# Kernel optimization log

Hardware: AMD Instinct MI355X
Metric: run time of the kernel (lower is better)

## Reference

```python
import jax, jax.numpy as jnp
import numpy as np

N_HEAD = 16
N_EMBD = 1024
HEAD_DIM = N_EMBD // N_HEAD
ROPE_BASE = 10000.0


def _rms_norm(x):
    # F.rms_norm with eps=None uses dtype eps
    eps = jnp.finfo(x.dtype).eps
    ms = jnp.mean(jnp.square(x), axis=-1, keepdims=True)
    return x * jax.lax.rsqrt(ms + eps)


def _rope_tables(T, dtype):
    inv_freq = 1.0 / (ROPE_BASE ** (jnp.arange(0, HEAD_DIM, 2, dtype=jnp.float32) / HEAD_DIM))
    t = jnp.arange(T, dtype=jnp.float32)
    freqs = jnp.outer(t, inv_freq)  # [T, D/2]
    cos = jnp.cos(freqs).astype(dtype)[None, :, None, :]  # [1,T,1,D/2]
    sin = jnp.sin(freqs).astype(dtype)[None, :, None, :]
    return cos, sin


def _apply_rotary(x, cos, sin):
    d = x.shape[-1] // 2
    x1, x2 = x[..., :d], x[..., d:]
    y1 = x1 * cos + x2 * sin
    y2 = -x1 * sin + x2 * cos
    return jnp.concatenate([y1, y2], axis=-1).astype(x.dtype)


def setup_inputs() -> dict:
    key = jax.random.key(0)
    ks = jax.random.split(key, 7)
    B, T, C = 4, 2048, N_EMBD
    s = 0.02
    return {
        "x": jax.random.normal(ks[0], (B, T, C), dtype=jnp.float32),
        "v1": jax.random.normal(ks[1], (B, T, C), dtype=jnp.float32),
        "Wq": jax.random.normal(ks[2], (C, C), dtype=jnp.float32) * s,
        "Wk": jax.random.normal(ks[3], (C, C), dtype=jnp.float32) * s,
        "Wv": jax.random.normal(ks[4], (C, C), dtype=jnp.float32) * s,
        "Wproj": jax.random.normal(ks[5], (C, C), dtype=jnp.float32) * s,
        "lamb": jnp.float32(0.5),
    }


def reference(x, v1, Wq, Wk, Wv, Wproj, lamb):
    B, T, C = x.shape
    H, D = N_HEAD, HEAD_DIM
    q = (x @ Wq.T).reshape(B, T, H, D)
    k = (x @ Wk.T).reshape(B, T, H, D)
    v = (x @ Wv.T).reshape(B, T, H, D)
    # value-lambda residual mix
    v = (1.0 - lamb) * v + lamb * v1.reshape(B, T, H, D)
    # RMSNorm then RoPE on q, k
    cos, sin = _rope_tables(T, x.dtype)
    q = _apply_rotary(_rms_norm(q), cos, sin)
    k = _apply_rotary(_rms_norm(k), cos, sin)
    # causal SDPA
    scale = 1.0 / jnp.sqrt(jnp.float32(D)).astype(x.dtype)
    scores = jnp.einsum("bthd,bshd->bhts", q, k) * scale  # [B,H,T,T]
    causal = jnp.tril(jnp.ones((T, T), dtype=bool))
    scores = jnp.where(causal[None, None], scores, jnp.finfo(scores.dtype).min)
    attn = jax.nn.softmax(scores, axis=-1)
    y = jnp.einsum("bhts,bshd->bthd", attn, v).reshape(B, T, C)
    y = y @ Wproj.T
    return (y, v1)
```

## Files before the change

kernel.cpp:

```cpp
#include <hip/hip_runtime.h>
#include <hip/hip_bf16.h>

typedef __bf16 bf16x8 __attribute__((ext_vector_type(8)));
typedef __bf16 bf16x4 __attribute__((ext_vector_type(4)));
typedef float  f32x4  __attribute__((ext_vector_type(4)));
typedef unsigned u32x4 __attribute__((ext_vector_type(4)));

#define B_ 4
#define T_ 2048
#define H_ 16
#define D_ 64
#define C_ 1024
#define M_ 8192
#define NE_ ((size_t)M_ * C_)

__global__ void probe_dtype(const unsigned short* __restrict__ x,
                            int* __restrict__ flag)
{
  __shared__ float red[256];
  float m = 0.0f;
  for (int i = threadIdx.x; i < 4096; i += 256) {
    unsigned int u = ((unsigned int)x[i]) << 16;
    float v = fabsf(__uint_as_float(u));
    if (!(v <= 1e30f)) v = 1e31f;
    m = fmaxf(m, v);
  }
  red[threadIdx.x] = m;
  __syncthreads();
  for (int s = 128; s > 0; s >>= 1) {
    if (threadIdx.x < s) red[threadIdx.x] = fmaxf(red[threadIdx.x], red[threadIdx.x + s]);
    __syncthreads();
  }
  if (threadIdx.x == 0) *flag = (red[0] > 100.0f) ? 1 : 0;
}

__device__ __forceinline__ float load1_adapt(const void* p, size_t idx, int f)
{
  if (f) return ((const float*)p)[idx];
  return __bfloat162float(((const __hip_bfloat16*)p)[idx]);
}

__global__ __launch_bounds__(256) void cvt_bf16(
    const int* __restrict__ flagp, const void* __restrict__ src,
    __bf16* __restrict__ dst, int n)
{
  const int f = *flagp;
  for (size_t i = ((size_t)blockIdx.x * 256 + threadIdx.x) * 8; i < (size_t)n;
       i += (size_t)gridDim.x * 2048) {
    bf16x8 r;
    if (f) {
      const float* pf = (const float*)src + i;
      float4 a = *(const float4*)pf;
      float4 b = *(const float4*)(pf + 4);
      r[0] = (__bf16)a.x; r[1] = (__bf16)a.y; r[2] = (__bf16)a.z; r[3] = (__bf16)a.w;
      r[4] = (__bf16)b.x; r[5] = (__bf16)b.y; r[6] = (__bf16)b.z; r[7] = (__bf16)b.w;
    } else {
      r = *(const bf16x8*)((const __bf16*)src + i);
    }
    *(bf16x8*)(dst + i) = r;
  }
}

__device__ __forceinline__ void g2lds16(const __bf16* g, __bf16* l)
{
  __builtin_amdgcn_global_load_lds(
      (const __attribute__((address_space(1))) void*)g,
      (__attribute__((address_space(3))) void*)l, 16, 0, 0);
}

__device__ __forceinline__ unsigned cvtpk_bf16(float lo, float hi)
{
  unsigned r;
  asm("v_cvt_pk_bf16_f32 %0, %1, %2" : "=v"(r) : "v"(lo), "v"(hi));
  return r;
}

__global__ __launch_bounds__(256) void gemm128(
    const __bf16* __restrict__ A, const __bf16* __restrict__ Bm,
    void* __restrict__ C, int M, int N, int K,
    const int* __restrict__ flagp, int adaptive)
{
  __shared__ __bf16 As[128][64];
  __shared__ __bf16 Bs[128][64];

  const int tid  = threadIdx.x;
  const int wv   = tid >> 6;
  const int lane = tid & 63;
  const int n16  = lane & 15;
  const int quad = lane >> 4;
  const int wm = (wv & 1) * 64, wn = (wv >> 1) * 64;

  const int nwgx = gridDim.x;
  const int id   = blockIdx.y * nwgx + blockIdx.x;
  const int cpx  = (nwgx * gridDim.y) >> 3;
  const int swz  = (id & 7) * cpx + (id >> 3);
  const int m0 = (swz % nwgx) * 128, n0 = (swz / nwgx) * 128;

  f32x4 acc[4][4];
#pragma unroll
  for (int i = 0; i < 4; i++)
#pragma unroll
    for (int j = 0; j < 4; j++) acc[i][j] = (f32x4){0.f, 0.f, 0.f, 0.f};

  const int trow = tid >> 3;
  const int tcol = (tid & 7) * 8;

  for (int k0 = 0; k0 < K; k0 += 64) {
#pragma unroll
    for (int p = 0; p < 4; p++) {
      g2lds16(A  + (size_t)(m0 + trow + p * 32) * K + k0 + tcol,
              &As[trow + p * 32][tcol]);
      g2lds16(Bm + (size_t)(n0 + trow + p * 32) * K + k0 + tcol,
              &Bs[trow + p * 32][tcol]);
    }
    __syncthreads();

#pragma unroll
    for (int kk = 0; kk < 2; kk++) {
      bf16x8 af[4], bf[4];
#pragma unroll
      for (int i = 0; i < 4; i++) {
        af[i] = *(const bf16x8*)&As[wm + i * 16 + n16][kk * 32 + quad * 8];
        bf[i] = *(const bf16x8*)&Bs[wn + i * 16 + n16][kk * 32 + quad * 8];
      }
#pragma unroll
      for (int i = 0; i < 4; i++)
#pragma unroll
        for (int j = 0; j < 4; j++)
          acc[i][j] = __builtin_amdgcn_mfma_f32_16x16x32_bf16(af[i], bf[j],
                                                              acc[i][j], 0, 0, 0);
    }
    __syncthreads();
  }

  const int f = adaptive ? *flagp : 0;
  const int rb = quad * 4;
#pragma unroll
  for (int i = 0; i < 4; i++)
#pragma unroll
    for (int j = 0; j < 4; j++)
#pragma unroll
      for (int r = 0; r < 4; r++) {
        const size_t idx = (size_t)(m0 + wm + i * 16 + rb + r) * N
                           + n0 + wn + j * 16 + n16;
        if (f) ((float*)C)[idx] = acc[i][j][r];
        else   ((__bf16*)C)[idx] = (__bf16)acc[i][j][r];
      }
}

__global__ __launch_bounds__(256) void fuse_rope_vmix(
    const int* __restrict__ flagp,
    __hip_bfloat16* __restrict__ q,
    __hip_bfloat16* __restrict__ k,
    __hip_bfloat16* __restrict__ v,
    const void* __restrict__ v1,
    const void* __restrict__ lambp)
{
  const int f    = *flagp;
  const int task = blockIdx.x * 4 + (threadIdx.x >> 6);
  const int lane = threadIdx.x & 63;
  const int h  = task & 15;
  const int bt = task >> 4;
  const int t  = bt & (T_ - 1);
  const size_t base = (size_t)bt * C_ + h * D_ + lane;

  const int j = lane & 31;
  const float inv = expf(-(float)j * (9.2103403719761836f / 32.0f));
  const float ang = (float)t * inv;
  const float cs = cosf(ang), sn = sinf(ang);
  const float EPS = 0.0078125f;

  {
    float xv = __bfloat162float(q[base]);
    float ss = xv * xv;
#pragma unroll
    for (int off = 32; off >= 1; off >>= 1) ss += __shfl_xor(ss, off);
    float r  = rsqrtf(ss * (1.0f / 64.0f) + EPS);
    float xn = xv * r;
    float pr = __shfl_xor(xn, 32);
    float yv = (lane < 32) ? (xn * cs + pr * sn) : (pr * -sn + xn * cs);
    q[base] = __float2bfloat16(yv);
  }
  {
    float xv = __bfloat162float(k[base]);
    float ss = xv * xv;
#pragma unroll
    for (int off = 32; off >= 1; off >>= 1) ss += __shfl_xor(ss, off);
    float r  = rsqrtf(ss * (1.0f / 64.0f) + EPS);
    float xn = xv * r;
    float pr = __shfl_xor(xn, 32);
    float yv = (lane < 32) ? (xn * cs + pr * sn) : (pr * -sn + xn * cs);
    k[base] = __float2bfloat16(yv);
  }
  {
    float lam = load1_adapt(lambp, 0, f);
    float vv  = __bfloat162float(v[base]);
    float v1v = load1_adapt(v1, base, f);
    v[base] = __float2bfloat16((1.0f - lam) * vv + lam * v1v);
  }
}

__global__ __launch_bounds__(256) void transp_v(
    const __bf16* __restrict__ v, __bf16* __restrict__ vt)
{
  __shared__ __bf16 Ts[64][72];
  const int bh = blockIdx.y;
  const int t0 = blockIdx.x * 64;
  const int b = bh >> 4, h = bh & 15;

  const int r = threadIdx.x >> 2;
  const int c = (threadIdx.x & 3) * 16;
  const __bf16* src = v + (size_t)(b * T_ + t0 + r) * C_ + h * D_ + c;
  *(bf16x8*)&Ts[r][c]     = *(const bf16x8*)src;
  *(bf16x8*)&Ts[r][c + 8] = *(const bf16x8*)(src + 8);
  __syncthreads();

  const int d  = threadIdx.x >> 2;
  const int tc = (threadIdx.x & 3) * 16;
  bf16x8 o0, o1;
#pragma unroll
  for (int jj = 0; jj < 8; jj++) { o0[jj] = Ts[tc + jj][d]; o1[jj] = Ts[tc + 8 + jj][d]; }
  __bf16* dst = vt + (size_t)(bh * D_ + d) * T_ + t0 + tc;
  *(bf16x8*)dst       = o0;
  *(bf16x8*)(dst + 8) = o1;
}

__global__ __launch_bounds__(256, 3) void attn_mfma(
    const __bf16* q,
    const __bf16* __restrict__ k,
    const __bf16* __restrict__ vt,
    __bf16* y)
{
  const int tid  = threadIdx.x;
  const int wv   = tid >> 6;
  const int lane = tid & 63;
  const int n16  = lane & 15;
  const int quad = lane >> 4;

  const int id = blockIdx.y * gridDim.x + blockIdx.x;
  const int bh = (id & 7) + 8 * ((id >> 3) & 7);
  const int bx = id >> 6;
  const int b = bh >> 4, h = bh & 15;
  const int q0 = (gridDim.x - 1 - bx) * 128;
  const size_t hb  = (size_t)b * T_ * C_ + h * D_;
  const size_t vhb = (size_t)bh * D_ * T_;

  bf16x8 aq[2][2];
#pragma unroll
  for (int rt = 0; rt < 2; rt++) {
    const size_t qoff = hb + (size_t)(q0 + wv * 32 + rt * 16 + n16) * C_;
    aq[rt][0] = *(const bf16x8*)(q + qoff + quad * 8);
    aq[rt][1] = *(const bf16x8*)(q + qoff + 32 + quad * 8);
#pragma unroll
    for (int jj = 0; jj < 8; jj++) {
      aq[rt][0][jj] = (__bf16)((float)aq[rt][0][jj] * 0.125f);
      aq[rt][1][jj] = (__bf16)((float)aq[rt][1][jj] * 0.125f);
    }
  }

  f32x4 Ot[2][4];
  float l_lane[2];
#pragma unroll
  for (int rt = 0; rt < 2; rt++) {
    l_lane[rt] = 0.0f;
#pragma unroll
    for (int t = 0; t < 4; t++) Ot[rt][t] = (f32x4){0.f, 0.f, 0.f, 0.f};
  }

  const int srcA = n16 + 32 * (quad & 1);
  const int srcB = srcA + 16;
  const bool lowq = quad < 2;

  const int rbase0 = q0 + wv * 32;
  const int niter  = (rbase0 + 31) / 64 + 1;

  for (int it = 0; it < niter; it++) {
    const int s0 = it * 64;

    bf16x8 kf[4][2], vf[4][2];
#pragma unroll
    for (int t = 0; t < 4; t++) {
      const __bf16* kp = k + hb + (size_t)(s0 + t * 16 + n16) * C_;
      kf[t][0] = *(const bf16x8*)(kp + quad * 8);
      kf[t][1] = *(const bf16x8*)(kp + 32 + quad * 8);
      const __bf16* vp = vt + vhb + (size_t)(t * 16 + n16) * T_ + s0;
      vf[t][0] = *(const bf16x8*)(vp + quad * 8);
      vf[t][1] = *(const bf16x8*)(vp + 32 + quad * 8);
    }

#pragma unroll
    for (int rt = 0; rt < 2; rt++) {
      const int rbase = rbase0 + rt * 16;
      if (s0 <= rbase + 15) {
        f32x4 S[4];
        __builtin_amdgcn_s_setprio(1);
#pragma unroll
        for (int t = 0; t < 4; t++) {
          S[t] = (f32x4){0.f, 0.f, 0.f, 0.f};
          S[t] = __builtin_amdgcn_mfma_f32_16x16x32_bf16(kf[t][0], aq[rt][0], S[t], 0, 0, 0);
          S[t] = __builtin_amdgcn_mfma_f32_16x16x32_bf16(kf[t][1], aq[rt][1], S[t], 0, 0, 0);
        }
        __builtin_amdgcn_s_setprio(0);

        if (s0 + 63 > rbase) {
          const int tg = rbase + n16;
#pragma unroll
          for (int t = 0; t < 4; t++) {
#pragma unroll
            for (int r = 0; r < 4; r++) {
              const int sg = s0 + t * 16 + quad * 4 + r;
              if (sg > tg) S[t][r] = -1e30f;
            }
          }
        }

        float p[4][4];
#pragma unroll
        for (int t = 0; t < 4; t++)
#pragma unroll
          for (int r = 0; r < 4; r++)
            p[t][r] = __expf(S[t][r] - 8.0f);
        l_lane[rt] += ((p[0][0] + p[0][1]) + (p[0][2] + p[0][3]))
                    + ((p[1][0] + p[1][1]) + (p[1][2] + p[1][3]))
                    + ((p[2][0] + p[2][1]) + (p[2][2] + p[2][3]))
                    + ((p[3][0] + p[3][1]) + (p[3][2] + p[3][3]));

        unsigned pk0[4], pk1[4];
#pragma unroll
        for (int t = 0; t < 4; t++) {
          pk0[t] = cvtpk_bf16(p[t][0], p[t][1]);
          pk1[t] = cvtpk_bf16(p[t][2], p[t][3]);
        }

        bf16x8 pf[2];
#pragma unroll
        for (int c = 0; c < 2; c++) {
          const int tE = 2 * c, tO = 2 * c + 1;
          unsigned a0 = (unsigned)__shfl((int)pk0[tE], srcA);
          unsigned a1 = (unsigned)__shfl((int)pk0[tO], srcA);
          unsigned b0 = (unsigned)__shfl((int)pk1[tE], srcA);
          unsigned b1 = (unsigned)__shfl((int)pk1[tO], srcA);
          unsigned c0 = (unsigned)__shfl((int)pk0[tE], srcB);
          unsigned c1 = (unsigned)__shfl((int)pk0[tO], srcB);
          unsigned d0 = (unsigned)__shfl((int)pk1[tE], srcB);
          unsigned d1 = (unsigned)__shfl((int)pk1[tO], srcB);
          union { u32x4 u; bf16x8 bv; } uw;
          uw.u[0] = lowq ? a0 : a1;
          uw.u[1] = lowq ? b0 : b1;
          uw.u[2] = lowq ? c0 : c1;
          uw.u[3] = lowq ? d0 : d1;
          pf[c] = uw.bv;
        }

        __builtin_amdgcn_s_setprio(1);
#pragma unroll
        for (int t = 0; t < 4; t++) {
          Ot[rt][t] = __builtin_amdgcn_mfma_f32_16x16x32_bf16(vf[t][0], pf[0], Ot[rt][t], 0, 0, 0);
          Ot[rt][t] = __builtin_amdgcn_mfma_f32_16x16x32_bf16(vf[t][1], pf[1], Ot[rt][t], 0, 0, 0);
        }
        __builtin_amdgcn_s_setprio(0);
      }
    }
  }

#pragma unroll
  for (int rt = 0; rt < 2; rt++) {
    float lt = l_lane[rt];
    lt += __shfl_xor(lt, 16);
    lt += __shfl_xor(lt, 32);
    const float linv = 1.0f / lt;
    const int qrow = q0 + wv * 32 + rt * 16 + n16;
#pragma unroll
    for (int t = 0; t < 4; t++) {
      bf16x4 o;
#pragma unroll
      for (int r = 0; r < 4; r++) o[r] = (__bf16)(Ot[rt][t][r] * linv);
      *(bf16x4*)(y + hb + (size_t)qrow * C_ + t * 16 + quad * 4) = o;
    }
  }
}

__global__ __launch_bounds__(256) void copy_v1(
    const int* __restrict__ flagp, const void* __restrict__ v1, void* __restrict__ out)
{
  const int f = *flagp;
  const size_t nbytes = NE_ * (f ? 4u : 2u);
  const uint4* s = (const uint4*)v1;
  uint4* d = (uint4*)((char*)out + nbytes);
  const size_t n16 = nbytes / 16;
  for (size_t i = (size_t)blockIdx.x * 256 + threadIdx.x; i < n16;
       i += (size_t)gridDim.x * 256)
    d[i] = s[i];
}

extern "C" void kernel_launch(void* const* d_in, const int* in_sizes, int n_in,
                              void* d_out, int out_size, void* d_ws, size_t ws_size,
                              hipStream_t stream)
{
  const void* x    = d_in[0];
  const void* v1   = d_in[1];
  const void* Wq   = d_in[2];
  const void* Wk   = d_in[3];
  const void* Wv   = d_in[4];
  const void* Wp   = d_in[5];
  const void* lamb = d_in[6];

  __bf16* xb  = (__bf16*)d_ws;
  __bf16* qw  = xb + NE_;
  __bf16* wqb = qw + NE_;
  __bf16* wkb = wqb + (size_t)C_ * C_;
  __bf16* wvb = wkb + (size_t)C_ * C_;
  __bf16* wpb = wvb + (size_t)C_ * C_;
  int* flagp  = (int*)(wpb + (size_t)C_ * C_);
  __bf16* vtb = xb;
  __bf16* kw = (__bf16*)d_out;
  __bf16* vw = (__bf16*)((char*)d_out + NE_ * 2);

  probe_dtype<<<1, 256, 0, stream>>>((const unsigned short*)x, flagp);

  cvt_bf16<<<4096, 256, 0, stream>>>(flagp, x,  xb,  (int)NE_);
  cvt_bf16<<<512,  256, 0, stream>>>(flagp, Wq, wqb, C_ * C_);
  cvt_bf16<<<512,  256, 0, stream>>>(flagp, Wk, wkb, C_ * C_);
  cvt_bf16<<<512,  256, 0, stream>>>(flagp, Wv, wvb, C_ * C_);
  cvt_bf16<<<512,  256, 0, stream>>>(flagp, Wp, wpb, C_ * C_);

  dim3 gg(M_ / 128, C_ / 128);
  gemm128<<<gg, 256, 0, stream>>>(xb, wqb, qw, M_, C_, C_, flagp, 0);
  gemm128<<<gg, 256, 0, stream>>>(xb, wkb, kw, M_, C_, C_, flagp, 0);
  gemm128<<<gg, 256, 0, stream>>>(xb, wvb, vw, M_, C_, C_, flagp, 0);

  fuse_rope_vmix<<<(M_ * H_) / 4, 256, 0, stream>>>(
      flagp, (__hip_bfloat16*)qw, (__hip_bfloat16*)kw, (__hip_bfloat16*)vw,
      v1, lamb);

  transp_v<<<dim3(T_ / 64, B_ * H_), 256, 0, stream>>>(vw, vtb);

  attn_mfma<<<dim3(T_ / 128, B_ * H_), 256, 0, stream>>>(qw, kw, vtb, qw);

  gemm128<<<gg, 256, 0, stream>>>(qw, wpb, d_out, M_, C_, C_, flagp, 1);
  copy_v1<<<8192, 256, 0, stream>>>(flagp, v1, d_out);
}
```

Baseline: 448.7 us.

## Fuse K/V projections into one GEMM and double-buffer attention K/V loads

Wk and Wv are assumed to sit next to each other in the workspace, so one GEMM with N=2048 produces an interleaved KV buffer with row stride 2048. The rope, transpose and attention kernels now index K and V with that stride. The attention loop is rewritten to prefetch the next 64-key K/V tile into a second register set while the current tile is computed, and launch bounds drop from 3 to 2 waves per SIMD to make room for the extra registers. This trades occupancy for load/compute overlap and saves one GEMM launch. It depends on wkb and wvb being contiguous, which holds for the existing workspace layout.

Result: no change. 452.3 us (+0.8%).

```diff
diff --git a/kernel.cpp b/kernel.cpp
--- a/kernel.cpp
+++ b/kernel.cpp
@@ -13,6 +13,7 @@
 #define C_ 1024
 #define M_ 8192
 #define NE_ ((size_t)M_ * C_)
+#define KVSTR_ 2048
 
 __global__ void probe_dtype(const unsigned short* __restrict__ x,
                             int* __restrict__ flag)
@@ -151,8 +152,7 @@
 __global__ __launch_bounds__(256) void fuse_rope_vmix(
     const int* __restrict__ flagp,
     __hip_bfloat16* __restrict__ q,
-    __hip_bfloat16* __restrict__ k,
-    __hip_bfloat16* __restrict__ v,
+    __hip_bfloat16* __restrict__ kv,
     const void* __restrict__ v1,
     const void* __restrict__ lambp)
 {
@@ -162,7 +162,8 @@
   const int h  = task & 15;
   const int bt = task >> 4;
   const int t  = bt & (T_ - 1);
-  const size_t base = (size_t)bt * C_ + h * D_ + lane;
+  const size_t baseq = (size_t)bt * C_ + h * D_ + lane;
+  const size_t basek = (size_t)bt * KVSTR_ + h * D_ + lane;
 
   const int j = lane & 31;
   const float inv = expf(-(float)j * (9.2103403719761836f / 32.0f));
@@ -171,7 +172,7 @@
   const float EPS = 0.0078125f;
 
   {
-    float xv = __bfloat162float(q[base]);
+    float xv = __bfloat162float(q[baseq]);
     float ss = xv * xv;
 #pragma unroll
     for (int off = 32; off >= 1; off >>= 1) ss += __shfl_xor(ss, off);
@@ -179,10 +180,10 @@
     float xn = xv * r;
     float pr = __shfl_xor(xn, 32);
     float yv = (lane < 32) ? (xn * cs + pr * sn) : (pr * -sn + xn * cs);
-    q[base] = __float2bfloat16(yv);
+    q[baseq] = __float2bfloat16(yv);
   }
   {
-    float xv = __bfloat162float(k[base]);
+    float xv = __bfloat162float(kv[basek]);
     float ss = xv * xv;
 #pragma unroll
     for (int off = 32; off >= 1; off >>= 1) ss += __shfl_xor(ss, off);
@@ -190,18 +191,18 @@
     float xn = xv * r;
     float pr = __shfl_xor(xn, 32);
     float yv = (lane < 32) ? (xn * cs + pr * sn) : (pr * -sn + xn * cs);
-    k[base] = __float2bfloat16(yv);
+    kv[basek] = __float2bfloat16(yv);
   }
   {
     float lam = load1_adapt(lambp, 0, f);
-    float vv  = __bfloat162float(v[base]);
-    float v1v = load1_adapt(v1, base, f);
-    v[base] = __float2bfloat16((1.0f - lam) * vv + lam * v1v);
+    float vv  = __bfloat162float(kv[basek + 1024]);
+    float v1v = load1_adapt(v1, baseq, f);
+    kv[basek + 1024] = __float2bfloat16((1.0f - lam) * vv + lam * v1v);
   }
 }
 
 __global__ __launch_bounds__(256) void transp_v(
-    const __bf16* __restrict__ v, __bf16* __restrict__ vt)
+    const __bf16* __restrict__ kv, __bf16* __restrict__ vt)
 {
   __shared__ __bf16 Ts[64][72];
   const int bh = blockIdx.y;
@@ -210,7 +211,7 @@
 
   const int r = threadIdx.x >> 2;
   const int c = (threadIdx.x & 3) * 16;
-  const __bf16* src = v + (size_t)(b * T_ + t0 + r) * C_ + h * D_ + c;
+  const __bf16* src = kv + (size_t)(b * T_ + t0 + r) * KVSTR_ + 1024 + h * D_ + c;
   *(bf16x8*)&Ts[r][c]     = *(const bf16x8*)src;
   *(bf16x8*)&Ts[r][c + 8] = *(const bf16x8*)(src + 8);
   __syncthreads();
@@ -225,9 +226,89 @@
   *(bf16x8*)(dst + 8) = o1;
 }
 
-__global__ __launch_bounds__(256, 3) void attn_mfma(
+__device__ __forceinline__ void attn_tile(
+    const bf16x8 (&KF)[4][2], const bf16x8 (&VF)[4][2],
+    const bf16x8 (&aq)[2][2], f32x4 (&Ot)[2][4], float (&l_lane)[2],
+    int s0, int rbase0, int n16, int quad, int srcA, int srcB, bool lowq)
+{
+#pragma unroll
+  for (int rt = 0; rt < 2; rt++) {
+    const int rbase = rbase0 + rt * 16;
+    if (s0 <= rbase + 15) {
+      f32x4 S[4];
+      __builtin_amdgcn_s_setprio(1);
+#pragma unroll
+      for (int t = 0; t < 4; t++) {
+        S[t] = (f32x4){0.f, 0.f, 0.f, 0.f};
+        S[t] = __builtin_amdgcn_mfma_f32_16x16x32_bf16(KF[t][0], aq[rt][0], S[t], 0, 0, 0);
+        S[t] = __builtin_amdgcn_mfma_f32_16x16x32_bf16(KF[t][1], aq[rt][1], S[t], 0, 0, 0);
+      }
+      __builtin_amdgcn_s_setprio(0);
+
+      if (s0 + 63 > rbase) {
+        const int tg = rbase + n16;
+#pragma unroll
+        for (int t = 0; t < 4; t++) {
+#pragma unroll
+          for (int r = 0; r < 4; r++) {
+            const int sg = s0 + t * 16 + quad * 4 + r;
+            if (sg > tg) S[t][r] = -1e30f;
+          }
+        }
+      }
+
+      float p[4][4];
+#pragma unroll
+      for (int t = 0; t < 4; t++)
+#pragma unroll
+        for (int r = 0; r < 4; r++)
+          p[t][r] = __expf(S[t][r] - 8.0f);
+      l_lane[rt] += ((p[0][0] + p[0][1]) + (p[0][2] + p[0][3]))
+                  + ((p[1][0] + p[1][1]) + (p[1][2] + p[1][3]))
+                  + ((p[2][0] + p[2][1]) + (p[2][2] + p[2][3]))
+                  + ((p[3][0] + p[3][1]) + (p[3][2] + p[3][3]));
+
+      unsigned pk0[4], pk1[4];
+#pragma unroll
+      for (int t = 0; t < 4; t++) {
+        pk0[t] = cvtpk_bf16(p[t][0], p[t][1]);
+        pk1[t] = cvtpk_bf16(p[t][2], p[t][3]);
+      }
+
+      bf16x8 pf[2];
+#pragma unroll
+      for (int c = 0; c < 2; c++) {
+        const int tE = 2 * c, tO = 2 * c + 1;
+        unsigned a0 = (unsigned)__shfl((int)pk0[tE], srcA);
+        unsigned a1 = (unsigned)__shfl((int)pk0[tO], srcA);
+        unsigned b0 = (unsigned)__shfl((int)pk1[tE], srcA);
+        unsigned b1 = (unsigned)__shfl((int)pk1[tO], srcA);
+        unsigned c0 = (unsigned)__shfl((int)pk0[tE], srcB);
+        unsigned c1 = (unsigned)__shfl((int)pk0[tO], srcB);
+        unsigned d0 = (unsigned)__shfl((int)pk1[tE], srcB);
+        unsigned d1 = (unsigned)__shfl((int)pk1[tO], srcB);
+        union { u32x4 u; bf16x8 bv; } uw;
+        uw.u[0] = lowq ? a0 : a1;
+        uw.u[1] = lowq ? b0 : b1;
+        uw.u[2] = lowq ? c0 : c1;
+        uw.u[3] = lowq ? d0 : d1;
+        pf[c] = uw.bv;
+      }
+
+      __builtin_amdgcn_s_setprio(1);
+#pragma unroll
+      for (int t = 0; t < 4; t++) {
+        Ot[rt][t] = __builtin_amdgcn_mfma_f32_16x16x32_bf16(VF[t][0], pf[0], Ot[rt][t], 0, 0, 0);
+        Ot[rt][t] = __builtin_amdgcn_mfma_f32_16x16x32_bf16(VF[t][1], pf[1], Ot[rt][t], 0, 0, 0);
+      }
+      __builtin_amdgcn_s_setprio(0);
+    }
+  }
+}
+
+__global__ __launch_bounds__(256, 2) void attn_mfma(
     const __bf16* q,
-    const __bf16* __restrict__ k,
+    const __bf16* __restrict__ kv,
     const __bf16* __restrict__ vt,
     __bf16* y)
 {
@@ -243,6 +324,7 @@
   const int b = bh >> 4, h = bh & 15;
   const int q0 = (gridDim.x - 1 - bx) * 128;
   const size_t hb  = (size_t)b * T_ * C_ + h * D_;
+  const size_t hbk = (size_t)b * T_ * KVSTR_ + h * D_;
   const size_t vhb = (size_t)bh * D_ * T_;
 
   bf16x8 aq[2][2];
@@ -274,94 +356,38 @@
   const int rbase0 = q0 + wv * 32;
   const int niter  = (rbase0 + 31) / 64 + 1;
 
-  for (int it = 0; it < niter; it++) {
-    const int s0 = it * 64;
-
-    bf16x8 kf[4][2], vf[4][2];
-#pragma unroll
-    for (int t = 0; t < 4; t++) {
-      const __bf16* kp = k + hb + (size_t)(s0 + t * 16 + n16) * C_;
-      kf[t][0] = *(const bf16x8*)(kp + quad * 8);
-      kf[t][1] = *(const bf16x8*)(kp + 32 + quad * 8);
-      const __bf16* vp = vt + vhb + (size_t)(t * 16 + n16) * T_ + s0;
-      vf[t][0] = *(const bf16x8*)(vp + quad * 8);
-      vf[t][1] = *(const bf16x8*)(vp + 32 + quad * 8);
-    }
-
-#pragma unroll
-    for (int rt = 0; rt < 2; rt++) {
-      const int rbase = rbase0 + rt * 16;
-      if (s0 <= rbase + 15) {
-        f32x4 S[4];
-        __builtin_amdgcn_s_setprio(1);
-#pragma unroll
-        for (int t = 0; t < 4; t++) {
-          S[t] = (f32x4){0.f, 0.f, 0.f, 0.f};
-          S[t] = __builtin_amdgcn_mfma_f32_16x16x32_bf16(kf[t][0], aq[rt][0], S[t], 0, 0, 0);
-          S[t] = __builtin_amdgcn_mfma_f32_16x16x32_bf16(kf[t][1], aq[rt][1], S[t], 0, 0, 0);
-        }
-        __builtin_amdgcn_s_setprio(0);
-
-        if (s0 + 63 > rbase) {
-          const int tg = rbase + n16;
-#pragma unroll
-          for (int t = 0; t < 4; t++) {
-#pragma unroll
-            for (int r = 0; r < 4; r++) {
-              const int sg = s0 + t * 16 + quad * 4 + r;
-              if (sg > tg) S[t][r] = -1e30f;
-            }
-          }
-        }
-
-        float p[4][4];
-#pragma unroll
-        for (int t = 0; t < 4; t++)
-#pragma unroll
-          for (int r = 0; r < 4; r++)
-            p[t][r] = __expf(S[t][r] - 8.0f);
-        l_lane[rt] += ((p[0][0] + p[0][1]) + (p[0][2] + p[0][3]))
-                    + ((p[1][0] + p[1][1]) + (p[1][2] + p[1][3]))
-                    + ((p[2][0] + p[2][1]) + (p[2][2] + p[2][3]))
-                    + ((p[3][0] + p[3][1]) + (p[3][2] + p[3][3]));
-
-        unsigned pk0[4], pk1[4];
-#pragma unroll
-        for (int t = 0; t < 4; t++) {
-          pk0[t] = cvtpk_bf16(p[t][0], p[t][1]);
-          pk1[t] = cvtpk_bf16(p[t][2], p[t][3]);
-        }
-
-        bf16x8 pf[2];
-#pragma unroll
-        for (int c = 0; c < 2; c++) {
-          const int tE = 2 * c, tO = 2 * c + 1;
-          unsigned a0 = (unsigned)__shfl((int)pk0[tE], srcA);
-          unsigned a1 = (unsigned)__shfl((int)pk0[tO], srcA);
-          unsigned b0 = (unsigned)__shfl((int)pk1[tE], srcA);
-          unsigned b1 = (unsigned)__shfl((int)pk1[tO], srcA);
-          unsigned c0 = (unsigned)__shfl((int)pk0[tE], srcB);
-          unsigned c1 = (unsigned)__shfl((int)pk0[tO], srcB);
-          unsigned d0 = (unsigned)__shfl((int)pk1[tE], srcB);
-          unsigned d1 = (unsigned)__shfl((int)pk1[tO], srcB);
-          union { u32x4 u; bf16x8 bv; } uw;
-          uw.u[0] = lowq ? a0 : a1;
-          uw.u[1] = lowq ? b0 : b1;
-          uw.u[2] = lowq ? c0 : c1;
-          uw.u[3] = lowq ? d0 : d1;
-          pf[c] = uw.bv;
-        }
-
-        __builtin_amdgcn_s_setprio(1);
-#pragma unroll
-        for (int t = 0; t < 4; t++) {
-          Ot[rt][t] = __builtin_amdgcn_mfma_f32_16x16x32_bf16(vf[t][0], pf[0], Ot[rt][t], 0, 0, 0);
-          Ot[rt][t] = __builtin_amdgcn_mfma_f32_16x16x32_bf16(vf[t][1], pf[1], Ot[rt][t], 0, 0, 0);
-        }
-        __builtin_amdgcn_s_setprio(0);
-      }
-    }
-  }
+#define LOADF(KF, VF, S0_)                                                   \
+  do {                                                                       \
+    _Pragma("unroll")                                                        \
+    for (int t = 0; t < 4; t++) {                                            \
+      const __bf16* kp = kv + hbk + (size_t)((S0_) + t * 16 + n16) * KVSTR_; \
+      KF[t][0] = *(const bf16x8*)(kp + quad * 8);                            \
+      KF[t][1] = *(const bf16x8*)(kp + 32 + quad * 8);                       \
+      const __bf16* vp = vt + vhb + (size_t)(t * 16 + n16) * T_ + (S0_);     \
+      VF[t][0] = *(const bf16x8*)(vp + quad * 8);                            \
+      VF[t][1] = *(const bf16x8*)(vp + 32 + quad * 8);                       \
+    }                                                                        \
+  } while (0)
+
+  bf16x8 kfA[4][2], vfA[4][2], kfB[4][2], vfB[4][2];
+  LOADF(kfA, vfA, 0);
+
+  int it = 0;
+  for (;;) {
+    int s0 = it * 64;
+    bool hn = (it + 1 < niter);
+    if (hn) LOADF(kfB, vfB, s0 + 64);
+    attn_tile(kfA, vfA, aq, Ot, l_lane, s0, rbase0, n16, quad, srcA, srcB, lowq);
+    if (!hn) break;
+    ++it;
+    s0 = it * 64;
+    hn = (it + 1 < niter);
+    if (hn) LOADF(kfA, vfA, s0 + 64);
+    attn_tile(kfB, vfB, aq, Ot, l_lane, s0, rbase0, n16, quad, srcA, srcB, lowq);
+    if (!hn) break;
+    ++it;
+  }
+#undef LOADF
 
 #pragma unroll
   for (int rt = 0; rt < 2; rt++) {
@@ -413,8 +439,7 @@
   __bf16* wpb = wvb + (size_t)C_ * C_;
   int* flagp  = (int*)(wpb + (size_t)C_ * C_);
   __bf16* vtb = xb;
-  __bf16* kw = (__bf16*)d_out;
-  __bf16* vw = (__bf16*)((char*)d_out + NE_ * 2);
+  __bf16* kvw = (__bf16*)d_out;
 
   probe_dtype<<<1, 256, 0, stream>>>((const unsigned short*)x, flagp);
 
@@ -424,19 +449,16 @@
   cvt_bf16<<<512,  256, 0, stream>>>(flagp, Wv, wvb, C_ * C_);
   cvt_bf16<<<512,  256, 0, stream>>>(flagp, Wp, wpb, C_ * C_);
 
-  dim3 gg(M_ / 128, C_ / 128);
-  gemm128<<<gg, 256, 0, stream>>>(xb, wqb, qw, M_, C_, C_, flagp, 0);
-  gemm128<<<gg, 256, 0, stream>>>(xb, wkb, kw, M_, C_, C_, flagp, 0);
-  gemm128<<<gg, 256, 0, stream>>>(xb, wvb, vw, M_, C_, C_, flagp, 0);
+  gemm128<<<dim3(M_ / 128, 8),  256, 0, stream>>>(xb, wqb, qw,  M_, 1024, C_, flagp, 0);
+  gemm128<<<dim3(M_ / 128, 16), 256, 0, stream>>>(xb, wkb, kvw, M_, 2048, C_, flagp, 0);
 
   fuse_rope_vmix<<<(M_ * H_) / 4, 256, 0, stream>>>(
-      flagp, (__hip_bfloat16*)qw, (__hip_bfloat16*)kw, (__hip_bfloat16*)vw,
-      v1, lamb);
-
-  transp_v<<<dim3(T_ / 64, B_ * H_), 256, 0, stream>>>(vw, vtb);
-
-  attn_mfma<<<dim3(T_ / 128, B_ * H_), 256, 0, stream>>>(qw, kw, vtb, qw);
-
-  gemm128<<<gg, 256, 0, stream>>>(qw, wpb, d_out, M_, C_, C_, flagp, 1);
+      flagp, (__hip_bfloat16*)qw, (__hip_bfloat16*)kvw, v1, lamb);
+
+  transp_v<<<dim3(T_ / 64, B_ * H_), 256, 0, stream>>>(kvw, vtb);
+
+  attn_mfma<<<dim3(T_ / 128, B_ * H_), 256, 0, stream>>>(qw, kvw, vtb, qw);
+
+  gemm128<<<dim3(M_ / 128, 8), 256, 0, stream>>>(qw, wpb, d_out, M_, 1024, C_, flagp, 1);
   copy_v1<<<8192, 256, 0, stream>>>(flagp, v1, d_out);
 }
```
